# Kernel tuning notes

Measured on AMD Instinct MI355X. Metric: run time of the kernel, lower is better.

The kernel has to match this reference:

```python
import jax, jax.numpy as jnp
import numpy as np

ITER_ROUTING = 3


def squash(t):
    # t: [..., H]
    norm = jnp.sum(t * t, axis=-1)                      # [...]
    scale = norm / (1.0 + norm)
    return scale[..., None] * t / jnp.sqrt(norm)[..., None]


def setup_inputs() -> dict:
    key = jax.random.key(0)
    k1, k2 = jax.random.split(key)
    C, K, H = 1024, 64, 512  # H = 2 * hidden_size, hidden_size = 256
    encoder_output = jax.random.normal(k1, (C, K, H), dtype=jnp.float32)
    # nn.Linear(H, H, bias=False): weight W has shape [H_out, H_in], y = x @ W.T
    W = jax.random.normal(k2, (H, H), dtype=jnp.float32) * (1.0 / np.sqrt(H))
    return {"encoder_output": encoder_output, "W": W}


def reference(encoder_output, W):
    C, K, H = encoder_output.shape
    # Linear projection is identical every iteration in the original loop;
    # compute once (same math, same values).
    x_hat = jnp.einsum('ckh,gh->ckg', encoder_output, W)  # [C, K, H]
    b = jnp.zeros((C, K), dtype=encoder_output.dtype)
    c = None
    for _ in range(ITER_ROUTING):
        d = jax.nn.softmax(b, axis=-1)                    # [C, K]
        c_hat = jnp.sum(x_hat * d[..., None], axis=1)     # [C, H]
        c = squash(c_hat)                                 # [C, H]
        b = b + jnp.einsum('ckh,ch->ck', x_hat, c)        # agreement update
    return c
```

## Files before the change

### kernel.cpp

```cpp
#include <hip/hip_runtime.h>
#include <math.h>


#define KC 64
#define HD 512
#define NT 512

typedef _Float16 half8  __attribute__((ext_vector_type(8)));
typedef _Float16 half4v __attribute__((ext_vector_type(4)));
typedef float    f32x4  __attribute__((ext_vector_type(4)));

__launch_bounds__(256)
__global__ void cast_w_kernel(const float* __restrict__ W, _Float16* __restrict__ W16) {
    int i = blockIdx.x * 256 + threadIdx.x;
    float4 v = reinterpret_cast<const float4*>(W)[i];
    half4v h = { (_Float16)v.x, (_Float16)v.y, (_Float16)v.z, (_Float16)v.w };
    reinterpret_cast<half4v*>(W16)[i] = h;
}

__launch_bounds__(NT, 4)
__global__ void routing_kernel(const float* __restrict__ enc,
                               const _Float16* __restrict__ W16,
                               float* __restrict__ out) {
    __shared__ _Float16 slab[2][8][64][8];
    __shared__ float chatL[HD];
    __shared__ float bvec[KC];
    __shared__ float dvec[KC];
    __shared__ float bpart[8][KC];
    __shared__ float red[8];
    __shared__ float s_alpha;

    const int tid  = threadIdx.x;
    const int lane = tid & 63;
    const int wave = tid >> 6;
    const int l15  = lane & 15, l4 = lane >> 4;
    const int c    = blockIdx.x;
    const float* ebase = enc + (size_t)c * (KC * HD);

    if (tid < KC) bvec[tid] = 0.0f;

    f32x4 acc[16];
    #pragma unroll
    for (int i = 0; i < 16; ++i) acc[i] = (f32x4){0.f, 0.f, 0.f, 0.f};

    auto stage = [&](int hs, int b) {
        #pragma unroll
        for (int j = 0; j < 2; ++j) {
            int idx = tid + (j << 9);
            int r   = idx >> 4;
            int c4  = (idx & 15) << 2;
            float4 v = *reinterpret_cast<const float4*>(ebase + (size_t)r * HD + hs * 64 + c4);
            half4v h = { (_Float16)v.x, (_Float16)v.y, (_Float16)v.z, (_Float16)v.w };
            int i2  = r >> 4;
            int ks  = c4 >> 5;
            int l4g = (c4 >> 3) & 3;
            int e0  = c4 & 7;
            *reinterpret_cast<half4v*>(&slab[b][i2 * 2 + ks][l4g * 16 + (r & 15)][e0]) = h;
        }
    };

    const _Float16* wb = W16 + (size_t)(wave * 64 + l15) * HD + l4 * 8;

    stage(0, 0);
    for (int hs = 0; hs < 8; ++hs) {
        __syncthreads();
        if (hs < 7) stage(hs + 1, (hs + 1) & 1);
        const int b = hs & 1;
        #pragma unroll
        for (int ks = 0; ks < 2; ++ks) {
            half8 bf[4], af[4];
            #pragma unroll
            for (int j = 0; j < 4; ++j)
                bf[j] = *reinterpret_cast<const half8*>(wb + j * (16 * HD) + hs * 64 + ks * 32);
            #pragma unroll
            for (int i = 0; i < 4; ++i)
                af[i] = *reinterpret_cast<const half8*>(&slab[b][i * 2 + ks][lane][0]);
            #pragma unroll
            for (int i = 0; i < 4; ++i)
                #pragma unroll
                for (int j = 0; j < 4; ++j)
                    acc[i * 4 + j] = __builtin_amdgcn_mfma_f32_16x16x32_f16(af[i], bf[j], acc[i * 4 + j], 0, 0, 0);
        }
    }
    __syncthreads();

    for (int it = 0; it < 3; ++it) {
        if (it > 0) {
            if (wave == 0) {
                float v = bvec[lane];
                float m = v;
                #pragma unroll
                for (int off = 32; off; off >>= 1) m = fmaxf(m, __shfl_xor(m, off));
                float e = expf(v - m);
                float s = e;
                #pragma unroll
                for (int off = 32; off; off >>= 1) s += __shfl_xor(s, off);
                dvec[lane] = e / s;
            }
            __syncthreads();
        }

        float chv[4];
        #pragma unroll
        for (int j = 0; j < 4; ++j) chv[j] = 0.f;
        #pragma unroll
        for (int i = 0; i < 4; ++i)
            #pragma unroll
            for (int r = 0; r < 4; ++r) {
                float dk = (it == 0) ? (1.0f / 64.0f) : dvec[i * 16 + l4 * 4 + r];
                #pragma unroll
                for (int j = 0; j < 4; ++j)
                    chv[j] += dk * acc[i * 4 + j][r];
            }
        #pragma unroll
        for (int j = 0; j < 4; ++j) {
            chv[j] += __shfl_xor(chv[j], 16);
            chv[j] += __shfl_xor(chv[j], 32);
        }
        if (l4 == 0) {
            #pragma unroll
            for (int j = 0; j < 4; ++j)
                chatL[wave * 64 + j * 16 + l15] = chv[j];
        }
        {
            float p = chv[0] * chv[0] + chv[1] * chv[1] + chv[2] * chv[2] + chv[3] * chv[3];
            #pragma unroll
            for (int off = 1; off <= 8; off <<= 1) p += __shfl_xor(p, off);
            if (lane == 0) red[wave] = p;
        }
        __syncthreads();
        if (tid == 0) {
            float n2 = red[0] + red[1] + red[2] + red[3] + red[4] + red[5] + red[6] + red[7];
            s_alpha = sqrtf(n2) / (1.0f + n2);
        }
        __syncthreads();

        if (it < 2) {
            #pragma unroll
            for (int i = 0; i < 4; ++i)
                #pragma unroll
                for (int r = 0; r < 4; ++r) {
                    float s = acc[i * 4 + 0][r] * chv[0]
                            + acc[i * 4 + 1][r] * chv[1]
                            + acc[i * 4 + 2][r] * chv[2]
                            + acc[i * 4 + 3][r] * chv[3];
                    #pragma unroll
                    for (int off = 1; off <= 8; off <<= 1) s += __shfl_xor(s, off);
                    if (l15 == 0) bpart[wave][i * 16 + l4 * 4 + r] = s;
                }
            __syncthreads();
            if (tid < KC) {
                float t = 0.f;
                #pragma unroll
                for (int w = 0; w < 8; ++w) t += bpart[w][tid];
                bvec[tid] += s_alpha * t;
            }
            __syncthreads();
        } else {
            out[(size_t)c * HD + tid] = s_alpha * chatL[tid];
        }
    }
}

extern "C" void kernel_launch(void* const* d_in, const int* in_sizes, int n_in,
                              void* d_out, int out_size, void* d_ws, size_t ws_size,
                              hipStream_t stream) {
    const float* enc = (const float*)d_in[0];
    const float* W   = (const float*)d_in[1];
    float* out       = (float*)d_out;
    _Float16* W16    = (_Float16*)d_ws;
    (void)in_sizes; (void)n_in; (void)ws_size; (void)out_size;

    cast_w_kernel<<<256, 256, 0, stream>>>(W, W16);
    routing_kernel<<<1024, NT, 0, stream>>>(enc, W16, out);
}
```

Baseline: 95.84 us.

## Pre-pack W into MFMA fragment order and register-prefetch encoder and weight tiles

The weight cast kernel now writes W in the exact per-lane MFMA B-fragment order, so each wave reads its fragments with contiguous coalesced 16-byte loads. The main loop issues global loads of the next encoder slab and next weight fragments into registers before the MFMAs and writes the slab to LDS afterwards, overlapping load latency with compute. LDS rows are XOR-swizzled to reduce bank conflicts, and launch bounds are relaxed to 2 blocks per CU to leave room for the extra prefetch registers, at the cost of possibly lower occupancy.

After: 81.15 us. 15.3% less time.

```diff
diff --git a/kernel.cpp b/kernel.cpp
--- a/kernel.cpp
+++ b/kernel.cpp
@@ -11,16 +11,25 @@
 typedef float    f32x4  __attribute__((ext_vector_type(4)));
 
 __launch_bounds__(256)
-__global__ void cast_w_kernel(const float* __restrict__ W, _Float16* __restrict__ W16) {
-    int i = blockIdx.x * 256 + threadIdx.x;
-    float4 v = reinterpret_cast<const float4*>(W)[i];
-    half4v h = { (_Float16)v.x, (_Float16)v.y, (_Float16)v.z, (_Float16)v.w };
-    reinterpret_cast<half4v*>(W16)[i] = h;
+__global__ void cast_w_kernel(const float* __restrict__ W, _Float16* __restrict__ Wp) {
+    int u    = blockIdx.x * 256 + threadIdx.x;
+    int lane = u & 63;
+    int j    = (u >> 6) & 3;
+    int ks   = (u >> 8) & 1;
+    int hs   = (u >> 9) & 7;
+    int wv   = (u >> 12) & 7;
+    int g  = wv * 64 + j * 16 + (lane & 15);
+    int h0 = hs * 64 + ks * 32 + (lane >> 4) * 8;
+    const float4* src = reinterpret_cast<const float4*>(W + (size_t)g * HD + h0);
+    float4 a = src[0], b = src[1];
+    half8 h = { (_Float16)a.x, (_Float16)a.y, (_Float16)a.z, (_Float16)a.w,
+                (_Float16)b.x, (_Float16)b.y, (_Float16)b.z, (_Float16)b.w };
+    *reinterpret_cast<half8*>(Wp + (size_t)u * 8) = h;
 }
 
-__launch_bounds__(NT, 4)
+__launch_bounds__(NT, 2)
 __global__ void routing_kernel(const float* __restrict__ enc,
-                               const _Float16* __restrict__ W16,
+                               const _Float16* __restrict__ Wp,
                                float* __restrict__ out) {
     __shared__ _Float16 slab[2][8][64][8];
     __shared__ float chatL[HD];
@@ -36,6 +45,7 @@
     const int l15  = lane & 15, l4 = lane >> 4;
     const int c    = blockIdx.x;
     const float* ebase = enc + (size_t)c * (KC * HD);
+    const _Float16* wbase = Wp + ((size_t)wave << 15) + (lane << 3);
 
     if (tid < KC) bvec[tid] = 0.0f;
 
@@ -43,44 +53,57 @@
     #pragma unroll
     for (int i = 0; i < 16; ++i) acc[i] = (f32x4){0.f, 0.f, 0.f, 0.f};
 
-    auto stage = [&](int hs, int b) {
-        #pragma unroll
-        for (int j = 0; j < 2; ++j) {
-            int idx = tid + (j << 9);
-            int r   = idx >> 4;
-            int c4  = (idx & 15) << 2;
-            float4 v = *reinterpret_cast<const float4*>(ebase + (size_t)r * HD + hs * 64 + c4);
-            half4v h = { (_Float16)v.x, (_Float16)v.y, (_Float16)v.z, (_Float16)v.w };
-            int i2  = r >> 4;
-            int ks  = c4 >> 5;
-            int l4g = (c4 >> 3) & 3;
-            int e0  = c4 & 7;
-            *reinterpret_cast<half4v*>(&slab[b][i2 * 2 + ks][l4g * 16 + (r & 15)][e0]) = h;
-        }
+    const int r0   = tid >> 4;
+    const int c40  = (tid & 15) << 2;
+    const int ks_w = c40 >> 5;
+    const int l4g  = (c40 >> 3) & 3;
+    const int e0w  = c40 & 7;
+    const int prow = (l4g * 16 + (r0 & 15)) ^ (l4g << 1);
+    const int p0   = (r0 >> 4) * 2 + ks_w;
+    const int p1   = p0 + 4;
+    const int plane_r = lane ^ ((lane >> 4) << 1);
+
+    float4 ev0, ev1;
+    auto eload = [&](int hs) {
+        ev0 = *reinterpret_cast<const float4*>(ebase + (size_t)r0 * HD + hs * 64 + c40);
+        ev1 = *reinterpret_cast<const float4*>(ebase + (size_t)(r0 + 32) * HD + hs * 64 + c40);
+    };
+    auto ewrite = [&](int b) {
+        half4v h0 = { (_Float16)ev0.x, (_Float16)ev0.y, (_Float16)ev0.z, (_Float16)ev0.w };
+        half4v h1 = { (_Float16)ev1.x, (_Float16)ev1.y, (_Float16)ev1.z, (_Float16)ev1.w };
+        *reinterpret_cast<half4v*>(&slab[b][p0][prow][e0w]) = h0;
+        *reinterpret_cast<half4v*>(&slab[b][p1][prow][e0w]) = h1;
     };
 
-    const _Float16* wb = W16 + (size_t)(wave * 64 + l15) * HD + l4 * 8;
+    half8 bf[2][8];
+    auto bload = [&](int hs) {
+        #pragma unroll
+        for (int q = 0; q < 8; ++q)
+            bf[hs & 1][q] = *reinterpret_cast<const half8*>(wbase + hs * 4096 + q * 512);
+    };
 
-    stage(0, 0);
+    bload(0);
+    eload(0);
+    ewrite(0);
+
+    #pragma unroll
     for (int hs = 0; hs < 8; ++hs) {
         __syncthreads();
-        if (hs < 7) stage(hs + 1, (hs + 1) & 1);
-        const int b = hs & 1;
+        if (hs < 7) { eload(hs + 1); bload(hs + 1); }
         #pragma unroll
         for (int ks = 0; ks < 2; ++ks) {
-            half8 bf[4], af[4];
-            #pragma unroll
-            for (int j = 0; j < 4; ++j)
-                bf[j] = *reinterpret_cast<const half8*>(wb + j * (16 * HD) + hs * 64 + ks * 32);
+            half8 af[4];
             #pragma unroll
             for (int i = 0; i < 4; ++i)
-                af[i] = *reinterpret_cast<const half8*>(&slab[b][i * 2 + ks][lane][0]);
+                af[i] = *reinterpret_cast<const half8*>(&slab[hs & 1][i * 2 + ks][plane_r][0]);
             #pragma unroll
             for (int i = 0; i < 4; ++i)
                 #pragma unroll
                 for (int j = 0; j < 4; ++j)
-                    acc[i * 4 + j] = __builtin_amdgcn_mfma_f32_16x16x32_f16(af[i], bf[j], acc[i * 4 + j], 0, 0, 0);
+                    acc[i * 4 + j] = __builtin_amdgcn_mfma_f32_16x16x32_f16(
+                        af[i], bf[hs & 1][ks * 4 + j], acc[i * 4 + j], 0, 0, 0);
         }
+        if (hs < 7) ewrite((hs + 1) & 1);
     }
     __syncthreads();
 
@@ -168,9 +191,9 @@
     const float* enc = (const float*)d_in[0];
     const float* W   = (const float*)d_in[1];
     float* out       = (float*)d_out;
-    _Float16* W16    = (_Float16*)d_ws;
+    _Float16* Wp     = (_Float16*)d_ws;
     (void)in_sizes; (void)n_in; (void)ws_size; (void)out_size;
 
-    cast_w_kernel<<<256, 256, 0, stream>>>(W, W16);
-    routing_kernel<<<1024, NT, 0, stream>>>(enc, W16, out);
+    cast_w_kernel<<<128, 256, 0, stream>>>(W, Wp);
+    routing_kernel<<<1024, NT, 0, stream>>>(enc, Wp, out);
 }
```
